# Performance work log

Measured on AMD Instinct MI355X. Metric: run time of the kernel, lower is better.

The kernel has to match this reference:

```python
import jax, jax.numpy as jnp
import numpy as np

_FIRST_DECODE_ID = 0  # _T5_DECODER_START_TOKEN_ID
B, L, V = 1, 520, 32128
REVIEW_INDEX = 512
LENIENCY = 2


def setup_inputs() -> dict:
    key = jax.random.key(0)
    k1, k2, k3 = jax.random.split(key, 3)
    target_logits = jax.random.normal(k1, (B, L, V), dtype=jnp.float32)
    probs = jax.random.uniform(k2, (B, L, V), dtype=jnp.float32)
    input_ids = jax.random.randint(k3, (B, L), 0, V, dtype=jnp.int64)
    return {
        "target_logits": target_logits,
        "probs": probs,
        "input_ids": input_ids,
        "review_index": REVIEW_INDEX,
        "leniency": LENIENCY,
    }


def reference(target_logits, probs, input_ids, review_index, leniency):
    r = int(review_index)
    L = input_ids.shape[1]
    K = L - r  # number of draft tokens under review

    target_probs = jax.nn.softmax(target_logits, axis=-1)          # (1, L, V)
    argmax_ids = jnp.argmax(target_probs, axis=-1)                  # (1, L)
    first = jnp.full((1, 1), _FIRST_DECODE_ID, dtype=input_ids.dtype)
    target_ids = jnp.concatenate([first, argmax_ids.astype(input_ids.dtype)], axis=-1)[:, r:]  # (1, K+1)
    target_probs_s = target_probs[:, r - 1:, :]                     # (1, K+1, V)
    probs_new = probs[:, r - 1:, :]                                 # (1, K+1, V)
    draft_ids = input_ids[:, r:]                                    # (1, K)

    # verification flags (fused replacement of the python early-exit loop)
    eq = target_ids[:, :K] == draft_ids                             # (1, K)
    tp = jnp.take_along_axis(target_probs_s[:, :K, :], draft_ids[..., None], axis=-1)[..., 0]
    pp = jnp.take_along_axis(probs_new[:, :K, :], draft_ids[..., None], axis=-1)[..., 0]
    lenient = (leniency > 1) & (tp > pp / jnp.float32(leniency))
    accept = eq | lenient                                           # (1, K)
    # n_match = length of leading run of accepts == match_ct in the loop
    n_match = jnp.sum(jnp.cumprod(accept.astype(jnp.int32), axis=-1))

    # id_res: prefix (r) + accepted drafts (n_match) + 1 bonus target token, padded to r+K+1
    pos = jnp.arange(K + 1)
    draft_pad = jnp.pad(draft_ids, ((0, 0), (0, 1)))                # (1, K+1)
    new_ids = jnp.where(pos < n_match, draft_pad[0],
                        jnp.where(pos == n_match, target_ids[0], 0))
    id_res = jnp.concatenate([input_ids[0, :r], new_ids])[None, :]  # (1, r+K+1)

    # prob_res: probs[:, :r] ++ target_probs of accepted positions, zero-padded to r+K
    mask = (jnp.arange(K) < n_match)[:, None]
    new_probs = jnp.where(mask, target_probs_s[0, :K, :], jnp.float32(0.0))
    prob_res = jnp.concatenate([probs[0, :r, :], new_probs], axis=0)[None]  # (1, r+K, V)

    return id_res, prob_res, n_match
```

## Files before the change

kernel.cpp:

```cpp
#include <hip/hip_runtime.h>
#include <hip/hip_bf16.h>


#define NCHUNK 32
#define RS_BLK 256

struct Ws {
    float pmax[16][NCHUNK];
    float psum[16][NCHUNK];
    int   pidx[16][NCHUNK];
    float mx[16];
    float sum[16];
    int   amax[16];
    int   n_match;
};

struct MIS { float m; int i; float s; };

__device__ inline MIS mis_merge(MIS a, MIS b) {
    MIS r;
    r.i = (b.m > a.m || (b.m == a.m && b.i < a.i)) ? b.i : a.i;
    r.m = fmaxf(a.m, b.m);
    r.s = 0.0f;
    if (a.s > 0.0f) r.s += a.s * expf(a.m - r.m);
    if (b.s > 0.0f) r.s += b.s * expf(b.m - r.m);
    return r;
}

__global__ void partial_stats_kernel(const float* __restrict__ logits, Ws* __restrict__ ws,
                                     int V, int row0) {
    int j  = blockIdx.y;
    int ch = blockIdx.x;
    int chunk_elems = V / NCHUNK;
    int nf4 = chunk_elems / 4;
    int cbase = ch * chunk_elems;
    const float4* row = (const float4*)(logits + (size_t)(row0 + j) * V + cbase);
    int t = threadIdx.x;

    float m = -INFINITY, s = 0.0f;
    int   idx = 0x7fffffff;
    for (int f = t; f < nf4; f += RS_BLK) {
        float4 v = row[f];
        float vv[4] = {v.x, v.y, v.z, v.w};
        int c = cbase + f * 4;
        #pragma unroll
        for (int u = 0; u < 4; u++) {
            float x = vv[u];
            if (x > m) { s = s * expf(m - x) + 1.0f; m = x; idx = c + u; }
            else       { s += expf(x - m); }
        }
    }

    __shared__ float sm[RS_BLK];
    __shared__ int   si[RS_BLK];
    __shared__ float ss[RS_BLK];
    sm[t] = m; si[t] = idx; ss[t] = s;
    __syncthreads();
    for (int w = RS_BLK >> 1; w > 0; w >>= 1) {
        if (t < w) {
            MIS a = {sm[t], si[t], ss[t]};
            MIS b = {sm[t + w], si[t + w], ss[t + w]};
            MIS r = mis_merge(a, b);
            sm[t] = r.m; si[t] = r.i; ss[t] = r.s;
        }
        __syncthreads();
    }
    if (t == 0) {
        ws->pmax[j][ch] = sm[0];
        ws->psum[j][ch] = ss[0];
        ws->pidx[j][ch] = si[0];
    }
}

__global__ void accept_kernel(const float* __restrict__ logits, const float* __restrict__ probs,
                              const int* __restrict__ ids, const int* __restrict__ leniency_p,
                              float* __restrict__ out, Ws* __restrict__ ws,
                              int V, int r, int K, long long out_last) {
    __shared__ int s_draft[16];
    __shared__ int s_acc[16];
    __shared__ int s_nm;
    int t = threadIdx.x;

    if (t <= K) {
        MIS acc = {ws->pmax[t][0], ws->pidx[t][0], ws->psum[t][0]};
        for (int c = 1; c < NCHUNK; c++) {
            MIS b = {ws->pmax[t][c], ws->pidx[t][c], ws->psum[t][c]};
            acc = mis_merge(acc, b);
        }
        ws->mx[t] = acc.m; ws->sum[t] = acc.s; ws->amax[t] = acc.i;
    }
    __syncthreads();

    for (int i = t; i < r; i += blockDim.x) out[i] = (float)ids[i];

    if (t < K) {
        int dj = ids[r + t];
        s_draft[t] = dj;
        size_t rowoff = (size_t)(r - 1 + t) * V;
        float tp = expf(logits[rowoff + dj] - ws->mx[t]) / ws->sum[t];
        float pp = probs[rowoff + dj];
        int   len = *leniency_p;
        bool eq      = (ws->amax[t] == dj);
        bool lenient = (len > 1) && (tp > pp / (float)len);
        s_acc[t] = (eq || lenient) ? 1 : 0;
    }
    __syncthreads();

    if (t == 0) {
        int nm = 0;
        for (int j = 0; j < K; j++) { if (s_acc[j]) nm++; else break; }
        s_nm = nm;
        ws->n_match = nm;
        out[out_last] = (float)nm;
    }
    __syncthreads();

    if (t <= K) {
        int pos = t;
        int nm  = s_nm;
        int v;
        if (pos < nm)       v = s_draft[pos];
        else if (pos == nm) v = ws->amax[pos];
        else                v = 0;
        out[r + pos] = (float)v;
    }
}

#define PW_BLK 256
#define PW_EPT 4

__global__ void write_probs_kernel(const float* __restrict__ logits, const float* __restrict__ probs,
                                   float* __restrict__ out, const Ws* __restrict__ ws,
                                   int V, int r, long long prob_off) {
    int y = blockIdx.y;
    long long ob = prob_off + (long long)y * V;
    int c0 = blockIdx.x * (PW_BLK * PW_EPT) + threadIdx.x;

    if (y < r) {
        const float* src = probs + (size_t)y * V;
        #pragma unroll
        for (int k = 0; k < PW_EPT; k++) {
            int c = c0 + k * PW_BLK;
            if (c < V) out[ob + c] = src[c];
        }
    } else {
        int j = y - r;
        int nm = ws->n_match;
        if (j < nm) {
            const float* lg = logits + (size_t)(r - 1 + j) * V;
            float m   = ws->mx[j];
            float inv = 1.0f / ws->sum[j];
            #pragma unroll
            for (int k = 0; k < PW_EPT; k++) {
                int c = c0 + k * PW_BLK;
                if (c < V) out[ob + c] = expf(lg[c] - m) * inv;
            }
        } else {
            #pragma unroll
            for (int k = 0; k < PW_EPT; k++) {
                int c = c0 + k * PW_BLK;
                if (c < V) out[ob + c] = 0.0f;
            }
        }
    }
}

extern "C" void kernel_launch(void* const* d_in, const int* in_sizes, int n_in,
                              void* d_out, int out_size, void* d_ws, size_t ws_size,
                              hipStream_t stream) {
    const float* logits     = (const float*)d_in[0];
    const float* probs      = (const float*)d_in[1];
    const int*   ids        = (const int*)d_in[2];
    const int*   leniency_p = (const int*)d_in[4];
    float* out = (float*)d_out;
    Ws*    ws  = (Ws*)d_ws;

    const int L = in_sizes[2];
    const int V = in_sizes[0] / L;
    const int r = 512;
    const int K = L - r;
    const long long prob_off = (long long)r + K + 1;
    const long long out_last = (long long)out_size - 1;

    dim3 g1(NCHUNK, K + 1, 1);
    partial_stats_kernel<<<g1, RS_BLK, 0, stream>>>(logits, ws, V, r - 1);

    accept_kernel<<<1, 512, 0, stream>>>(logits, probs, ids, leniency_p, out, ws,
                                         V, r, K, out_last);

    int gx = (V + PW_BLK * PW_EPT - 1) / (PW_BLK * PW_EPT);
    dim3 grid(gx, L, 1);
    write_probs_kernel<<<grid, PW_BLK, 0, stream>>>(logits, probs, out, ws, V, r, prob_off);
}
```

Baseline: 38.51 us.

## Fuse probs prefix copy into stats kernel and vectorize the copy

Moves the large copy of the first r probability rows out of the final write kernel and into the same launch as the softmax partial-statistics blocks. The copy therefore no longer waits on the serial accept kernel and can run alongside the stats reduction. The copy also uses 16-byte vector stores, with a 3-element offset chosen to match the output alignment. The final kernel now only writes the K tail rows. This adds index bookkeeping and relies on an unaligned-load vector type for the source.

Result: faster. 34.79 us (-9.7%).

```diff
diff --git a/kernel.cpp b/kernel.cpp
--- a/kernel.cpp
+++ b/kernel.cpp
@@ -3,7 +3,8 @@
 
 
 #define NCHUNK 32
-#define RS_BLK 256
+#define BLK 256
+#define CP_EPT 8
 
 struct Ws {
     float pmax[16][NCHUNK];
@@ -27,41 +28,71 @@
     return r;
 }
 
-__global__ void partial_stats_kernel(const float* __restrict__ logits, Ws* __restrict__ ws,
-                                     int V, int row0) {
-    int j  = blockIdx.y;
-    int ch = blockIdx.x;
+typedef float f4u __attribute__((ext_vector_type(4), aligned(4)));
+
+__global__ void fused_copy_stats(const float* __restrict__ logits,
+                                 const float* __restrict__ probs,
+                                 float* __restrict__ out, Ws* __restrict__ ws,
+                                 int V, int row0, long long prob_off,
+                                 int nCopyBlocks, int blocksPerRow, int nf4) {
+    int t = threadIdx.x;
+
+    if ((int)blockIdx.x < nCopyBlocks) {
+        int y   = blockIdx.x / blocksPerRow;
+        int sub = blockIdx.x % blocksPerRow;
+        const float* src = probs + (size_t)y * V;
+        float*       dst = out + prob_off + (size_t)y * V;
+
+        if (sub == 0) {
+            if (t < 3)       dst[t] = src[t];
+            else if (t == 3) dst[V - 1] = src[V - 1];
+        }
+        int f0 = sub * (BLK * CP_EPT) + t;
+        #pragma unroll
+        for (int k = 0; k < CP_EPT; k++) {
+            int f = f0 + k * BLK;
+            if (f < nf4) {
+                f4u v = *reinterpret_cast<const f4u*>(src + 3 + 4 * f);
+                *reinterpret_cast<float4*>(dst + 3 + 4 * f) =
+                    float4{v.x, v.y, v.z, v.w};
+            }
+        }
+        return;
+    }
+
+    int idx = blockIdx.x - nCopyBlocks;
+    int ch = idx & (NCHUNK - 1);
+    int j  = idx / NCHUNK;
     int chunk_elems = V / NCHUNK;
-    int nf4 = chunk_elems / 4;
+    int cf4 = chunk_elems / 4;
     int cbase = ch * chunk_elems;
     const float4* row = (const float4*)(logits + (size_t)(row0 + j) * V + cbase);
-    int t = threadIdx.x;
 
     float m = -INFINITY, s = 0.0f;
-    int   idx = 0x7fffffff;
-    for (int f = t; f < nf4; f += RS_BLK) {
+    int   mi = 0x7fffffff;
+    for (int f = t; f < cf4; f += BLK) {
         float4 v = row[f];
         float vv[4] = {v.x, v.y, v.z, v.w};
         int c = cbase + f * 4;
         #pragma unroll
         for (int u = 0; u < 4; u++) {
             float x = vv[u];
-            if (x > m) { s = s * expf(m - x) + 1.0f; m = x; idx = c + u; }
+            if (x > m) { s = s * expf(m - x) + 1.0f; m = x; mi = c + u; }
             else       { s += expf(x - m); }
         }
     }
 
-    __shared__ float sm[RS_BLK];
-    __shared__ int   si[RS_BLK];
-    __shared__ float ss[RS_BLK];
-    sm[t] = m; si[t] = idx; ss[t] = s;
-    __syncthreads();
-    for (int w = RS_BLK >> 1; w > 0; w >>= 1) {
+    __shared__ float sm[BLK];
+    __shared__ int   si[BLK];
+    __shared__ float ss[BLK];
+    sm[t] = m; si[t] = mi; ss[t] = s;
+    __syncthreads();
+    for (int w = BLK >> 1; w > 0; w >>= 1) {
         if (t < w) {
             MIS a = {sm[t], si[t], ss[t]};
             MIS b = {sm[t + w], si[t + w], ss[t + w]};
-            MIS r = mis_merge(a, b);
-            sm[t] = r.m; si[t] = r.i; ss[t] = r.s;
+            MIS rr = mis_merge(a, b);
+            sm[t] = rr.m; si[t] = rr.i; ss[t] = rr.s;
         }
         __syncthreads();
     }
@@ -116,9 +147,7 @@
     __syncthreads();
 
     if (t <= K) {
-        int pos = t;
-        int nm  = s_nm;
-        int v;
+        int pos = t, nm = s_nm, v;
         if (pos < nm)       v = s_draft[pos];
         else if (pos == nm) v = ws->amax[pos];
         else                v = 0;
@@ -126,41 +155,30 @@
     }
 }
 
-#define PW_BLK 256
-#define PW_EPT 4
-
-__global__ void write_probs_kernel(const float* __restrict__ logits, const float* __restrict__ probs,
-                                   float* __restrict__ out, const Ws* __restrict__ ws,
-                                   int V, int r, long long prob_off) {
-    int y = blockIdx.y;
-    long long ob = prob_off + (long long)y * V;
-    int c0 = blockIdx.x * (PW_BLK * PW_EPT) + threadIdx.x;
-
-    if (y < r) {
-        const float* src = probs + (size_t)y * V;
-        #pragma unroll
-        for (int k = 0; k < PW_EPT; k++) {
-            int c = c0 + k * PW_BLK;
-            if (c < V) out[ob + c] = src[c];
+#define TP_EPT 4
+
+__global__ void tail_probs_kernel(const float* __restrict__ logits,
+                                  float* __restrict__ out, const Ws* __restrict__ ws,
+                                  int V, int r, long long prob_off) {
+    int j = blockIdx.y;
+    long long ob = prob_off + (long long)(r + j) * V;
+    int c0 = blockIdx.x * (BLK * TP_EPT) + threadIdx.x;
+    int nm = ws->n_match;
+
+    if (j < nm) {
+        const float* lg = logits + (size_t)(r - 1 + j) * V;
+        float m   = ws->mx[j];
+        float inv = 1.0f / ws->sum[j];
+        #pragma unroll
+        for (int k = 0; k < TP_EPT; k++) {
+            int c = c0 + k * BLK;
+            if (c < V) out[ob + c] = expf(lg[c] - m) * inv;
         }
     } else {
-        int j = y - r;
-        int nm = ws->n_match;
-        if (j < nm) {
-            const float* lg = logits + (size_t)(r - 1 + j) * V;
-            float m   = ws->mx[j];
-            float inv = 1.0f / ws->sum[j];
-            #pragma unroll
-            for (int k = 0; k < PW_EPT; k++) {
-                int c = c0 + k * PW_BLK;
-                if (c < V) out[ob + c] = expf(lg[c] - m) * inv;
-            }
-        } else {
-            #pragma unroll
-            for (int k = 0; k < PW_EPT; k++) {
-                int c = c0 + k * PW_BLK;
-                if (c < V) out[ob + c] = 0.0f;
-            }
+        #pragma unroll
+        for (int k = 0; k < TP_EPT; k++) {
+            int c = c0 + k * BLK;
+            if (c < V) out[ob + c] = 0.0f;
         }
     }
 }
@@ -182,13 +200,17 @@
     const long long prob_off = (long long)r + K + 1;
     const long long out_last = (long long)out_size - 1;
 
-    dim3 g1(NCHUNK, K + 1, 1);
-    partial_stats_kernel<<<g1, RS_BLK, 0, stream>>>(logits, ws, V, r - 1);
+    const int nf4 = (V - 4) / 4;
+    const int blocksPerRow = (nf4 + BLK * CP_EPT - 1) / (BLK * CP_EPT);
+    const int nCopyBlocks  = r * blocksPerRow;
+    const int nStatsBlocks = (K + 1) * NCHUNK;
+
+    fused_copy_stats<<<nCopyBlocks + nStatsBlocks, BLK, 0, stream>>>(
+        logits, probs, out, ws, V, r - 1, prob_off, nCopyBlocks, blocksPerRow, nf4);
 
     accept_kernel<<<1, 512, 0, stream>>>(logits, probs, ids, leniency_p, out, ws,
                                          V, r, K, out_last);
 
-    int gx = (V + PW_BLK * PW_EPT - 1) / (PW_BLK * PW_EPT);
-    dim3 grid(gx, L, 1);
-    write_probs_kernel<<<grid, PW_BLK, 0, stream>>>(logits, probs, out, ws, V, r, prob_off);
-}
+    dim3 g3((V + BLK * TP_EPT - 1) / (BLK * TP_EPT), K, 1);
+    tail_probs_kernel<<<g3, BLK, 0, stream>>>(logits, out, ws, V, r, prob_off);
+}
```
